# Kernel optimization log

Measured on AMD Instinct MI355X. Metric: run time of the kernel, lower is better.

Reference implementation:

```python
import jax, jax.numpy as jnp
import numpy as np

N_NODES = 100000


def gcn_conv(x, src, dst, W, b, n_nodes):
    """PyG GCNConv: out = D^{-1/2} (A + I) D^{-1/2} X W + b (self-loops added)."""
    h = x @ W  # [N, out]
    loops = jnp.arange(n_nodes, dtype=src.dtype)
    s = jnp.concatenate([src, loops])
    d = jnp.concatenate([dst, loops])
    deg = jax.ops.segment_sum(jnp.ones_like(d, dtype=h.dtype), d, num_segments=n_nodes)
    dinv = jnp.where(deg > 0, jax.lax.rsqrt(deg), 0.0)
    norm = dinv[s] * dinv[d]  # [E+N]
    msgs = norm[:, None] * h[s]  # gather + scale
    out = jax.ops.segment_sum(msgs, d, num_segments=n_nodes)
    return out + b


def setup_inputs() -> dict:
    key = jax.random.key(0)
    ks = jax.random.split(key, 10)
    n, e, f_in = N_NODES, 1600000, 128
    x = jax.random.normal(ks[0], (n, f_in), dtype=jnp.float32)
    edge_index = jax.random.randint(ks[1], (2, e), 0, n, dtype=jnp.int64)
    dims = [f_in, 15, 20, 27, 36]
    params = {}
    for i in range(4):
        fan_in, fan_out = dims[i], dims[i + 1]
        scale = 1.0 / np.sqrt(fan_in)
        params[f"W{i+1}"] = jax.random.uniform(ks[2 + 2 * i], (fan_in, fan_out), minval=-scale, maxval=scale, dtype=jnp.float32)
        params[f"b{i+1}"] = jax.random.uniform(ks[3 + 2 * i], (fan_out,), minval=-scale, maxval=scale, dtype=jnp.float32)
    return {"x": x, "edge_index": edge_index, **params}


def reference(x, edge_index, W1, b1, W2, b2, W3, b3, W4, b4):
    src, dst = edge_index[0], edge_index[1]
    n = x.shape[0]
    h = jax.nn.selu(gcn_conv(x, src, dst, W1, b1, n))
    h = jax.nn.selu(gcn_conv(h, src, dst, W2, b2, n))
    h = jax.nn.selu(gcn_conv(h, src, dst, W3, b3, n))
    h = jax.nn.selu(gcn_conv(h, src, dst, W4, b4, n))
    return h
```

## Files before the change

### kernel.cpp

```cpp
#include <hip/hip_runtime.h>
#include <hip/hip_fp16.h>
#include <math.h>

#define BLK 256
#define CBSH 9
#define CBN 512
#define NCBC 256
#define NB2 512

__device__ __forceinline__ float selu_f(float x) {
    const float kScale = 1.0507009873554805f;
    const float kAlpha = 1.6732632423543772f;
    return x > 0.0f ? kScale * x : kScale * kAlpha * expm1f(x);
}

__device__ __forceinline__ float2 h2f2(unsigned u) {
    __half2 h = *reinterpret_cast<__half2*>(&u);
    return __half22float2(h);
}
__device__ __forceinline__ void h8_set(float* a, uint4 v) {
    float2 f0 = h2f2(v.x), f1 = h2f2(v.y), f2 = h2f2(v.z), f3 = h2f2(v.w);
    a[0] = f0.x; a[1] = f0.y; a[2] = f1.x; a[3] = f1.y;
    a[4] = f2.x; a[5] = f2.y; a[6] = f3.x; a[7] = f3.y;
}
__device__ __forceinline__ void h8_add(float* a, uint4 v) {
    float2 f0 = h2f2(v.x), f1 = h2f2(v.y), f2 = h2f2(v.z), f3 = h2f2(v.w);
    a[0] += f0.x; a[1] += f0.y; a[2] += f1.x; a[3] += f1.y;
    a[4] += f2.x; a[5] += f2.y; a[6] += f3.x; a[7] += f3.y;
}

__global__ void k_cnt(const int* __restrict__ dst, int* __restrict__ H, int e, int nbkt) {
    __shared__ int hist[NCBC];
    int tid = threadIdx.x;
    for (int b = tid; b < nbkt; b += BLK) hist[b] = 0;
    __syncthreads();
    int per = (e + NB2 - 1) / NB2;
    int lo = blockIdx.x * per;
    int hi = min(e, lo + per);
    for (int i = lo + tid; i < hi; i += BLK) atomicAdd(&hist[dst[i] >> CBSH], 1);
    __syncthreads();
    for (int b = tid; b < nbkt; b += BLK) H[blockIdx.x * nbkt + b] = hist[b];
}

__global__ void k_bsum(const int* __restrict__ H, int* __restrict__ bstart, int nbkt, int e) {
    __shared__ int tot[NCBC];
    int tid = threadIdx.x;
    for (int b = tid; b < nbkt; b += BLK) {
        int s = 0;
        for (int i = 0; i < NB2; ++i) s += H[i * nbkt + b];
        tot[b] = s;
    }
    __syncthreads();
    if (tid == 0) {
        int acc = 0;
        for (int b = 0; b < nbkt; ++b) {
            bstart[b] = acc;
            acc += tot[b];
        }
        bstart[nbkt] = acc;
    }
}

__global__ void k_off(int* __restrict__ H, const int* __restrict__ bstart, int nbkt) {
    __shared__ int lds[BLK];
    int b = blockIdx.x, tid = threadIdx.x;
    int v0 = H[(2 * tid) * nbkt + b];
    int v1 = H[(2 * tid + 1) * nbkt + b];
    int pair = v0 + v1;
    lds[tid] = pair;
    __syncthreads();
    int val = pair;
    for (int off = 1; off < BLK; off <<= 1) {
        int t2 = (tid >= off) ? lds[tid - off] : 0;
        __syncthreads();
        val += t2;
        lds[tid] = val;
        __syncthreads();
    }
    int excl = val - pair + bstart[b];
    H[(2 * tid) * nbkt + b] = excl;
    H[(2 * tid + 1) * nbkt + b] = excl + v0;
}

__global__ void k_scatter2(const int* __restrict__ src, const int* __restrict__ dst,
                           const int* __restrict__ H, unsigned* __restrict__ slab,
                           int e, int nbkt) {
    __shared__ int cur[NCBC];
    int tid = threadIdx.x;
    for (int b = tid; b < nbkt; b += BLK) cur[b] = H[blockIdx.x * nbkt + b];
    __syncthreads();
    int per = (e + NB2 - 1) / NB2;
    int lo = blockIdx.x * per;
    int hi = min(e, lo + per);
    for (int i = lo + tid; i < hi; i += BLK) {
        int s = src[i], d = dst[i];
        int b = d >> CBSH;
        int pos = atomicAdd(&cur[b], 1);
        slab[pos] = ((unsigned)s << CBSH) | (unsigned)(d & (CBN - 1));
    }
}

__global__ void k_build(const int* __restrict__ bstart, const unsigned* __restrict__ slab,
                        int* __restrict__ rowptr, float* __restrict__ dinv,
                        int* __restrict__ csr, int n, int e) {
    __shared__ int hist[CBN];
    __shared__ int stmp[BLK];
    int b = blockIdx.x, tid = threadIdx.x;
    hist[2 * tid] = 0;
    hist[2 * tid + 1] = 0;
    __syncthreads();
    int lo = bstart[b], hi = bstart[b + 1];
    for (int i = lo + tid; i < hi; i += BLK) atomicAdd(&hist[slab[i] & (CBN - 1)], 1);
    __syncthreads();
    int h0 = hist[2 * tid], h1 = hist[2 * tid + 1];
    int pair = h0 + h1;
    stmp[tid] = pair;
    __syncthreads();
    int val = pair;
    for (int off = 1; off < BLK; off <<= 1) {
        int t2 = (tid >= off) ? stmp[tid - off] : 0;
        __syncthreads();
        val += t2;
        stmp[tid] = val;
        __syncthreads();
    }
    int e0 = lo + val - pair;
    int e1 = e0 + h0;
    hist[2 * tid] = e0;
    hist[2 * tid + 1] = e1;
    int node0 = b << CBSH;
    int nA = node0 + 2 * tid, nB = nA + 1;
    if (nA < n) { rowptr[nA] = e0; dinv[nA] = rsqrtf((float)(h0 + 1)); }
    if (nB < n) { rowptr[nB] = e1; dinv[nB] = rsqrtf((float)(h1 + 1)); }
    if (b == 0 && tid == 0) rowptr[n] = e;
    __syncthreads();
    for (int i = lo + tid; i < hi; i += BLK) {
        unsigned p = slab[i];
        int pos = atomicAdd(&hist[p & (CBN - 1)], 1);
        csr[pos] = (int)(p >> CBSH);
    }
}

template <int K, int KP, int F, int SI, int SO, bool FUSE_IN>
__global__ void k_gemm(const float* __restrict__ xin, const float* __restrict__ W,
                       const float* __restrict__ bprev, const float* __restrict__ dinv,
                       __half* __restrict__ hs, int n) {
    constexpr int F8 = (F + 7) & ~7;
    int i = blockIdx.x * BLK + threadIdx.x;
    if (i >= n) return;
    const float* xr = xin + (size_t)i * SI;
    float di = dinv[i];
    float accf[F8];
#pragma unroll
    for (int f = 0; f < F8; ++f) accf[f] = 0.0f;
#pragma unroll
    for (int k4 = 0; k4 < KP / 4; ++k4) {
        float4 xv = *reinterpret_cast<const float4*>(xr + k4 * 4);
        float xs4[4] = {xv.x, xv.y, xv.z, xv.w};
#pragma unroll
        for (int j = 0; j < 4; ++j) {
            const int k = k4 * 4 + j;
            if (k < K) {
                float xval = xs4[j];
                if (FUSE_IN) xval = selu_f(di * xval + bprev[k]);
#pragma unroll
                for (int f = 0; f < F; ++f) accf[f] = fmaf(xval, W[k * F + f], accf[f]);
            }
        }
    }
#pragma unroll
    for (int f = 0; f < F; ++f) accf[f] *= di;
    __half2* ro2 = reinterpret_cast<__half2*>(hs + (size_t)i * SO);
#pragma unroll
    for (int f2 = 0; f2 < F8 / 2; ++f2)
        ro2[f2] = __float22half2_rn(make_float2(accf[2 * f2], accf[2 * f2 + 1]));
}

template <int F, int S , int ACT, int NPN, int SOUT, bool LAST>
__global__ void k_agg(const int* __restrict__ rowptr, const int* __restrict__ csr,
                      const __half* __restrict__ hs, float* __restrict__ out,
                      const float* __restrict__ dinv, const float* __restrict__ bias,
                      int n) {
    int lane = threadIdx.x & 63;
    int g = lane / ACT;
    int fl = lane - g * ACT;
    int wid = (blockIdx.x * BLK + threadIdx.x) >> 6;
    int d = wid * NPN + g;
    if (g >= NPN || d >= n) return;
    int beg = rowptr[d], end = rowptr[d + 1];
    auto rowp = [&](int r) {
        return reinterpret_cast<const uint4*>(hs + (size_t)r * S) + fl;
    };
    float s0[8], s1[8] = {0}, s2[8] = {0}, s3[8] = {0};
    h8_set(s0, *rowp(d));
    int p = beg;
    for (; p + 8 <= end; p += 8) {
        int e0 = __builtin_nontemporal_load(csr + p);
        int e1 = __builtin_nontemporal_load(csr + p + 1);
        int e2 = __builtin_nontemporal_load(csr + p + 2);
        int e3 = __builtin_nontemporal_load(csr + p + 3);
        int e4 = __builtin_nontemporal_load(csr + p + 4);
        int e5 = __builtin_nontemporal_load(csr + p + 5);
        int e6 = __builtin_nontemporal_load(csr + p + 6);
        int e7 = __builtin_nontemporal_load(csr + p + 7);
        uint4 v0 = *rowp(e0), v1 = *rowp(e1), v2 = *rowp(e2), v3 = *rowp(e3);
        uint4 v4 = *rowp(e4), v5 = *rowp(e5), v6 = *rowp(e6), v7 = *rowp(e7);
        h8_add(s0, v0); h8_add(s1, v1); h8_add(s2, v2); h8_add(s3, v3);
        h8_add(s0, v4); h8_add(s1, v5); h8_add(s2, v6); h8_add(s3, v7);
    }
    for (; p + 4 <= end; p += 4) {
        int e0 = __builtin_nontemporal_load(csr + p);
        int e1 = __builtin_nontemporal_load(csr + p + 1);
        int e2 = __builtin_nontemporal_load(csr + p + 2);
        int e3 = __builtin_nontemporal_load(csr + p + 3);
        uint4 v0 = *rowp(e0), v1 = *rowp(e1), v2 = *rowp(e2), v3 = *rowp(e3);
        h8_add(s0, v0); h8_add(s1, v1); h8_add(s2, v2); h8_add(s3, v3);
    }
    for (; p < end; ++p) h8_add(s0, *rowp(__builtin_nontemporal_load(csr + p)));
    float sum[8];
#pragma unroll
    for (int j = 0; j < 8; ++j) sum[j] = (s0[j] + s1[j]) + (s2[j] + s3[j]);
    if (LAST) {
        float dv = dinv[d];
        float r[8];
#pragma unroll
        for (int j = 0; j < 8; ++j) {
            int col = fl * 8 + j;
            r[j] = (col < F) ? selu_f(dv * sum[j] + bias[col]) : 0.0f;
        }
        float* op = out + (size_t)d * F + fl * 8;
        *reinterpret_cast<float4*>(op) = make_float4(r[0], r[1], r[2], r[3]);
        if (fl * 8 + 4 < F)
            *reinterpret_cast<float4*>(op + 4) = make_float4(r[4], r[5], r[6], r[7]);
    } else {
        float* op = out + (size_t)d * SOUT + fl * 8;
        *reinterpret_cast<float4*>(op) = make_float4(sum[0], sum[1], sum[2], sum[3]);
        *reinterpret_cast<float4*>(op + 4) = make_float4(sum[4], sum[5], sum[6], sum[7]);
    }
}

extern "C" void kernel_launch(void* const* d_in, const int* in_sizes, int n_in,
                              void* d_out, int out_size, void* d_ws, size_t ws_size,
                              hipStream_t stream) {
    const float* x = (const float*)d_in[0];
    const int* ei = (const int*)d_in[1];
    const float* W1 = (const float*)d_in[2];
    const float* b1 = (const float*)d_in[3];
    const float* W2 = (const float*)d_in[4];
    const float* b2 = (const float*)d_in[5];
    const float* W3 = (const float*)d_in[6];
    const float* b3 = (const float*)d_in[7];
    const float* W4 = (const float*)d_in[8];
    const float* b4 = (const float*)d_in[9];

    int n = in_sizes[0] / 128;
    int e = in_sizes[1] / 2;
    const int* s32 = ei;
    const int* d32 = ei + e;
    int nbkt = (n + CBN - 1) >> CBSH;

    char* w = (char*)d_ws;
    auto alloc = [&](size_t bytes) {
        char* p = w;
        w += (bytes + 255) & ~(size_t)255;
        return p;
    };
    int* rowptr = (int*)alloc(((size_t)n + 1) * 4);
    float* dinv = (float*)alloc((size_t)n * 4);
    int* csr = (int*)alloc((size_t)e * 4);
    int* H = (int*)alloc((size_t)NB2 * nbkt * 4);
    int* bstart = (int*)alloc(((size_t)nbkt + 1) * 4);
    __half* bufA = (__half*)alloc((size_t)n * 40 * 2);
    float* bufB = (float*)alloc((size_t)n * 32 * 4);
    unsigned* slab = (unsigned*)bufA;

    int nb = (n + BLK - 1) / BLK;

    k_cnt<<<NB2, BLK, 0, stream>>>(d32, H, e, nbkt);
    k_bsum<<<1, BLK, 0, stream>>>(H, bstart, nbkt, e);
    k_off<<<nbkt, BLK, 0, stream>>>(H, bstart, nbkt);
    k_scatter2<<<NB2, BLK, 0, stream>>>(s32, d32, H, slab, e, nbkt);
    k_build<<<nbkt, BLK, 0, stream>>>(bstart, slab, rowptr, dinv, csr, n, e);

    int ab1 = (n + 127) / 128;
    int ab2 = (n + 83) / 84;
    int ab3 = (n + 63) / 64;
    int ab4 = (n + 47) / 48;

    k_gemm<128, 128, 15, 128, 16, false><<<nb, BLK, 0, stream>>>(x, W1, nullptr, dinv, bufA, n);
    k_agg<15, 16, 2, 32, 16, false><<<ab1, BLK, 0, stream>>>(rowptr, csr, bufA, bufB, dinv, nullptr, n);

    k_gemm<15, 16, 20, 16, 32, true><<<nb, BLK, 0, stream>>>(bufB, W2, b1, dinv, bufA, n);
    k_agg<20, 32, 3, 21, 32, false><<<ab2, BLK, 0, stream>>>(rowptr, csr, bufA, bufB, dinv, nullptr, n);

    k_gemm<20, 20, 27, 32, 32, true><<<nb, BLK, 0, stream>>>(bufB, W3, b2, dinv, bufA, n);
    k_agg<27, 32, 4, 16, 32, false><<<ab3, BLK, 0, stream>>>(rowptr, csr, bufA, bufB, dinv, nullptr, n);

    k_gemm<27, 28, 36, 32, 40, true><<<nb, BLK, 0, stream>>>(bufB, W4, b3, dinv, bufA, n);
    k_agg<36, 40, 5, 12, 36, true><<<ab4, BLK, 0, stream>>>(rowptr, csr, bufA, (float*)d_out, dinv, b4, n);
}
```

Baseline: 271.5 us.

## Fuse each aggregation with the next layer's GEMM through shared memory

Layers 2-4 no longer use a separate aggregation pass that writes fp32 sums and a GEMM pass that rereads them. A combined kernel gathers neighbour rows, applies bias and SELU, stages the activated row in LDS, multiplies by the next weight matrix, and writes the scaled fp16 result directly. This removes three launches and the fp32 intermediate round trip through memory. The cost is a block-wide barrier and extra register and LDS pressure in the gather kernel, and the GEMM work is spread unevenly across lanes.

```diff
diff --git a/kernel.cpp b/kernel.cpp
--- a/kernel.cpp
+++ b/kernel.cpp
@@ -27,6 +27,18 @@
     float2 f0 = h2f2(v.x), f1 = h2f2(v.y), f2 = h2f2(v.z), f3 = h2f2(v.w);
     a[0] += f0.x; a[1] += f0.y; a[2] += f1.x; a[3] += f1.y;
     a[4] += f2.x; a[5] += f2.y; a[6] += f3.x; a[7] += f3.y;
+}
+__device__ __forceinline__ uint4 f8_pack(const float* a) {
+    __half2 h0 = __float22half2_rn(make_float2(a[0], a[1]));
+    __half2 h1 = __float22half2_rn(make_float2(a[2], a[3]));
+    __half2 h2 = __float22half2_rn(make_float2(a[4], a[5]));
+    __half2 h3 = __float22half2_rn(make_float2(a[6], a[7]));
+    uint4 u;
+    u.x = *reinterpret_cast<unsigned*>(&h0);
+    u.y = *reinterpret_cast<unsigned*>(&h1);
+    u.z = *reinterpret_cast<unsigned*>(&h2);
+    u.w = *reinterpret_cast<unsigned*>(&h3);
+    return u;
 }
 
 __global__ void k_cnt(const int* __restrict__ dst, int* __restrict__ H, int e, int nbkt) {
@@ -141,46 +153,122 @@
     }
 }
 
-template <int K, int KP, int F, int SI, int SO, bool FUSE_IN>
-__global__ void k_gemm(const float* __restrict__ xin, const float* __restrict__ W,
-                       const float* __restrict__ bprev, const float* __restrict__ dinv,
-                       __half* __restrict__ hs, int n) {
-    constexpr int F8 = (F + 7) & ~7;
+__global__ void k_gemm1(const float* __restrict__ xin, const float* __restrict__ W,
+                        const float* __restrict__ dinv, __half* __restrict__ hs, int n) {
     int i = blockIdx.x * BLK + threadIdx.x;
     if (i >= n) return;
-    const float* xr = xin + (size_t)i * SI;
-    float di = dinv[i];
-    float accf[F8];
-#pragma unroll
-    for (int f = 0; f < F8; ++f) accf[f] = 0.0f;
-#pragma unroll
-    for (int k4 = 0; k4 < KP / 4; ++k4) {
+    const float* xr = xin + (size_t)i * 128;
+    float accf[16];
+#pragma unroll
+    for (int f = 0; f < 16; ++f) accf[f] = 0.0f;
+#pragma unroll
+    for (int k4 = 0; k4 < 32; ++k4) {
         float4 xv = *reinterpret_cast<const float4*>(xr + k4 * 4);
         float xs4[4] = {xv.x, xv.y, xv.z, xv.w};
 #pragma unroll
         for (int j = 0; j < 4; ++j) {
             const int k = k4 * 4 + j;
+#pragma unroll
+            for (int f = 0; f < 15; ++f) accf[f] = fmaf(xs4[j], W[k * 15 + f], accf[f]);
+        }
+    }
+    float di = dinv[i];
+#pragma unroll
+    for (int f = 0; f < 15; ++f) accf[f] *= di;
+    accf[15] = 0.0f;
+    __half2* ro2 = reinterpret_cast<__half2*>(hs + (size_t)i * 16);
+#pragma unroll
+    for (int f2 = 0; f2 < 8; ++f2)
+        ro2[f2] = __float22half2_rn(make_float2(accf[2 * f2], accf[2 * f2 + 1]));
+}
+
+template <int CHI, int NPN, int SIN, int K, int KP, int FN, int CHO, int SON>
+__global__ void k_aggemm(const int* __restrict__ rowptr, const int* __restrict__ csr,
+                         const __half* __restrict__ hsin, const float* __restrict__ bprev,
+                         const float* __restrict__ dinv, const float* __restrict__ W,
+                         __half* __restrict__ hsout, int n) {
+    __shared__ float xl[4][NPN][KP];
+    int lane = threadIdx.x & 63;
+    int wv = threadIdx.x >> 6;
+    int g = lane / CHI;
+    int fl = lane - g * CHI;
+    int wid = (blockIdx.x * BLK + threadIdx.x) >> 6;
+    int d = wid * NPN + g;
+    bool active = (g < NPN) && (d < n);
+    if (active) {
+        int beg = rowptr[d], end = rowptr[d + 1];
+        auto rowp = [&](int r) {
+            return reinterpret_cast<const uint4*>(hsin + (size_t)r * SIN) + fl;
+        };
+        float s0[8], s1[8] = {0}, s2[8] = {0}, s3[8] = {0};
+        h8_set(s0, *rowp(d));
+        int p = beg;
+        for (; p + 8 <= end; p += 8) {
+            int e0 = __builtin_nontemporal_load(csr + p);
+            int e1 = __builtin_nontemporal_load(csr + p + 1);
+            int e2 = __builtin_nontemporal_load(csr + p + 2);
+            int e3 = __builtin_nontemporal_load(csr + p + 3);
+            int e4 = __builtin_nontemporal_load(csr + p + 4);
+            int e5 = __builtin_nontemporal_load(csr + p + 5);
+            int e6 = __builtin_nontemporal_load(csr + p + 6);
+            int e7 = __builtin_nontemporal_load(csr + p + 7);
+            uint4 v0 = *rowp(e0), v1 = *rowp(e1), v2 = *rowp(e2), v3 = *rowp(e3);
+            uint4 v4 = *rowp(e4), v5 = *rowp(e5), v6 = *rowp(e6), v7 = *rowp(e7);
+            h8_add(s0, v0); h8_add(s1, v1); h8_add(s2, v2); h8_add(s3, v3);
+            h8_add(s0, v4); h8_add(s1, v5); h8_add(s2, v6); h8_add(s3, v7);
+        }
+        for (; p + 4 <= end; p += 4) {
+            int e0 = __builtin_nontemporal_load(csr + p);
+            int e1 = __builtin_nontemporal_load(csr + p + 1);
+            int e2 = __builtin_nontemporal_load(csr + p + 2);
+            int e3 = __builtin_nontemporal_load(csr + p + 3);
+            uint4 v0 = *rowp(e0), v1 = *rowp(e1), v2 = *rowp(e2), v3 = *rowp(e3);
+            h8_add(s0, v0); h8_add(s1, v1); h8_add(s2, v2); h8_add(s3, v3);
+        }
+        for (; p < end; ++p) h8_add(s0, *rowp(__builtin_nontemporal_load(csr + p)));
+        float di = dinv[d];
+#pragma unroll
+        for (int j = 0; j < 8; ++j) {
+            int k = fl * 8 + j;
             if (k < K) {
-                float xval = xs4[j];
-                if (FUSE_IN) xval = selu_f(di * xval + bprev[k]);
-#pragma unroll
-                for (int f = 0; f < F; ++f) accf[f] = fmaf(xval, W[k * F + f], accf[f]);
+                float s = (s0[j] + s1[j]) + (s2[j] + s3[j]);
+                xl[wv][g][k] = selu_f(di * s + bprev[k]);
             }
         }
     }
-#pragma unroll
-    for (int f = 0; f < F; ++f) accf[f] *= di;
-    __half2* ro2 = reinterpret_cast<__half2*>(hs + (size_t)i * SO);
-#pragma unroll
-    for (int f2 = 0; f2 < F8 / 2; ++f2)
-        ro2[f2] = __float22half2_rn(make_float2(accf[2 * f2], accf[2 * f2 + 1]));
-}
-
-template <int F, int S , int ACT, int NPN, int SOUT, bool LAST>
-__global__ void k_agg(const int* __restrict__ rowptr, const int* __restrict__ csr,
-                      const __half* __restrict__ hs, float* __restrict__ out,
-                      const float* __restrict__ dinv, const float* __restrict__ bias,
-                      int n) {
+    __syncthreads();
+    if (active) {
+        float di = dinv[d];
+#pragma unroll
+        for (int c = fl; c < CHO; c += CHI) {
+            float acc[8];
+#pragma unroll
+            for (int j = 0; j < 8; ++j) acc[j] = 0.0f;
+#pragma unroll
+            for (int k = 0; k < K; ++k) {
+                float xv = xl[wv][g][k];
+#pragma unroll
+                for (int j = 0; j < 8; ++j) {
+                    int col = c * 8 + j;
+                    if (col < FN) acc[j] = fmaf(xv, W[k * FN + col], acc[j]);
+                }
+            }
+            float gg[8];
+#pragma unroll
+            for (int j = 0; j < 8; ++j) {
+                int col = c * 8 + j;
+                gg[j] = (col < FN) ? di * acc[j] : 0.0f;
+            }
+            *reinterpret_cast<uint4*>(hsout + (size_t)d * SON + c * 8) = f8_pack(gg);
+        }
+    }
+}
+
+template <int F, int S, int ACT, int NPN>
+__global__ void k_aggL(const int* __restrict__ rowptr, const int* __restrict__ csr,
+                       const __half* __restrict__ hs, float* __restrict__ out,
+                       const float* __restrict__ dinv, const float* __restrict__ bias,
+                       int n) {
     int lane = threadIdx.x & 63;
     int g = lane / ACT;
     int fl = lane - g * ACT;
@@ -217,26 +305,18 @@
         h8_add(s0, v0); h8_add(s1, v1); h8_add(s2, v2); h8_add(s3, v3);
     }
     for (; p < end; ++p) h8_add(s0, *rowp(__builtin_nontemporal_load(csr + p)));
-    float sum[8];
-#pragma unroll
-    for (int j = 0; j < 8; ++j) sum[j] = (s0[j] + s1[j]) + (s2[j] + s3[j]);
-    if (LAST) {
-        float dv = dinv[d];
-        float r[8];
-#pragma unroll
-        for (int j = 0; j < 8; ++j) {
-            int col = fl * 8 + j;
-            r[j] = (col < F) ? selu_f(dv * sum[j] + bias[col]) : 0.0f;
-        }
-        float* op = out + (size_t)d * F + fl * 8;
-        *reinterpret_cast<float4*>(op) = make_float4(r[0], r[1], r[2], r[3]);
-        if (fl * 8 + 4 < F)
-            *reinterpret_cast<float4*>(op + 4) = make_float4(r[4], r[5], r[6], r[7]);
-    } else {
-        float* op = out + (size_t)d * SOUT + fl * 8;
-        *reinterpret_cast<float4*>(op) = make_float4(sum[0], sum[1], sum[2], sum[3]);
-        *reinterpret_cast<float4*>(op + 4) = make_float4(sum[4], sum[5], sum[6], sum[7]);
-    }
+    float dv = dinv[d];
+    float r[8];
+#pragma unroll
+    for (int j = 0; j < 8; ++j) {
+        int col = fl * 8 + j;
+        float s = (s0[j] + s1[j]) + (s2[j] + s3[j]);
+        r[j] = (col < F) ? selu_f(dv * s + bias[col]) : 0.0f;
+    }
+    float* op = out + (size_t)d * F + fl * 8;
+    *reinterpret_cast<float4*>(op) = make_float4(r[0], r[1], r[2], r[3]);
+    if (fl * 8 + 4 < F)
+        *reinterpret_cast<float4*>(op + 4) = make_float4(r[4], r[5], r[6], r[7]);
 }
 
 extern "C" void kernel_launch(void* const* d_in, const int* in_sizes, int n_in,
@@ -271,7 +351,7 @@
     int* H = (int*)alloc((size_t)NB2 * nbkt * 4);
     int* bstart = (int*)alloc(((size_t)nbkt + 1) * 4);
     __half* bufA = (__half*)alloc((size_t)n * 40 * 2);
-    float* bufB = (float*)alloc((size_t)n * 32 * 4);
+    __half* bufC = (__half*)alloc((size_t)n * 40 * 2);
     unsigned* slab = (unsigned*)bufA;
 
     int nb = (n + BLK - 1) / BLK;
@@ -287,15 +367,16 @@
     int ab3 = (n + 63) / 64;
     int ab4 = (n + 47) / 48;
 
-    k_gemm<128, 128, 15, 128, 16, false><<<nb, BLK, 0, stream>>>(x, W1, nullptr, dinv, bufA, n);
-    k_agg<15, 16, 2, 32, 16, false><<<ab1, BLK, 0, stream>>>(rowptr, csr, bufA, bufB, dinv, nullptr, n);
-
-    k_gemm<15, 16, 20, 16, 32, true><<<nb, BLK, 0, stream>>>(bufB, W2, b1, dinv, bufA, n);
-    k_agg<20, 32, 3, 21, 32, false><<<ab2, BLK, 0, stream>>>(rowptr, csr, bufA, bufB, dinv, nullptr, n);
-
-    k_gemm<20, 20, 27, 32, 32, true><<<nb, BLK, 0, stream>>>(bufB, W3, b2, dinv, bufA, n);
-    k_agg<27, 32, 4, 16, 32, false><<<ab3, BLK, 0, stream>>>(rowptr, csr, bufA, bufB, dinv, nullptr, n);
-
-    k_gemm<27, 28, 36, 32, 40, true><<<nb, BLK, 0, stream>>>(bufB, W4, b3, dinv, bufA, n);
-    k_agg<36, 40, 5, 12, 36, true><<<ab4, BLK, 0, stream>>>(rowptr, csr, bufA, (float*)d_out, dinv, b4, n);
-}
+    k_gemm1<<<nb, BLK, 0, stream>>>(x, W1, dinv, bufA, n);
+
+    k_aggemm<2, 32, 16, 15, 17, 20, 3, 32><<<ab1, BLK, 0, stream>>>(
+        rowptr, csr, bufA, b1, dinv, W2, bufC, n);
+
+    k_aggemm<3, 21, 32, 20, 21, 27, 4, 32><<<ab2, BLK, 0, stream>>>(
+        rowptr, csr, bufC, b2, dinv, W3, bufA, n);
+
+    k_aggemm<4, 16, 32, 27, 29, 36, 5, 40><<<ab3, BLK, 0, stream>>>(
+        rowptr, csr, bufA, b3, dinv, W4, bufC, n);
+
+    k_aggL<36, 40, 5, 12><<<ab4, BLK, 0, stream>>>(rowptr, csr, bufC, (float*)d_out, dinv, b4, n);
+}
```

Result: faster. 260.5 us (-4.1%).
